# Optimization experiments

Hardware: AMD Instinct MI355X
Metric: run time of the kernel (lower is better)

## Reference

```python
import jax, jax.numpy as jnp
import numpy as np

N_BINS = 256
HOP = 80


def _gru(xs, Wih, Whh, bih, bhh, reverse=False):
    """Single-layer unidirectional GRU, PyTorch gate layout (r, z, n).
    xs: (T, B, I); Wih: (3H, I); Whh: (3H, H). Returns (T, B, H)."""
    H = Whh.shape[1]
    gi = jnp.einsum('tbi,gi->tbg', xs, Wih) + bih  # precompute input projections

    def step(h, gi_t):
        gh = h @ Whh.T + bhh
        ir, iz, inn = jnp.split(gi_t, 3, axis=-1)
        hr, hz, hn = jnp.split(gh, 3, axis=-1)
        r = jax.nn.sigmoid(ir + hr)
        z = jax.nn.sigmoid(iz + hz)
        n = jnp.tanh(inn + r * hn)
        h_new = (1.0 - z) * n + z * h
        return h_new, h_new

    h0 = jnp.zeros((xs.shape[1], H), xs.dtype)
    _, ys = jax.lax.scan(step, h0, gi, reverse=reverse)
    return ys


def _quantize(w):
    # continuous [-1, 1] -> bin index in [0, N_BINS-1]
    return jnp.clip(jnp.floor((w + 1.0) * (N_BINS / 2)), 0, N_BINS - 1).astype(jnp.int32)


def _forward(x, y, p):
    # --- encode: 2-layer bidirectional GRU over mel frames ---
    c = x
    for l in ('m0', 'm1'):
        f = _gru(c, p[l + 'f_Wih'], p[l + 'f_Whh'], p[l + 'f_bih'], p[l + 'f_bhh'])
        bwd = _gru(c, p[l + 'b_Wih'], p[l + 'b_Whh'], p[l + 'b_bih'], p[l + 'b_bhh'], reverse=True)
        c = jnp.concatenate([f, bwd], axis=-1)  # (t_m, b, 2*dim_enc)
    # nearest-neighbor upsample in time (matches F.interpolate default 'nearest')
    c = jnp.repeat(c, HOP, axis=0)  # (t_w, b, 2*dim_enc)

    # --- teacher forcing: shift waveform right, vectorize via embedding ---
    b = x.shape[1]
    w = jnp.concatenate([jnp.zeros((1, b), y.dtype), y[:-1]], axis=0)
    e = p['E'][_quantize(w)]  # (t_w, b, dim_vec)

    # --- wav GRU + projection + GELU ---
    o = _gru(jnp.concatenate([e, c], axis=-1), p['w_Wih'], p['w_Whh'], p['w_bih'], p['w_bhh'])
    o = jax.nn.gelu(o @ p['Wp'].T + p['bp'], approximate=False)  # (t_w, b, dim_proj)

    # --- categorical neg log prob over quantized targets ---
    logits = o @ p['Wd'].T + p['bd']  # (t_w, b, N_BINS)
    logp = jax.nn.log_softmax(logits, axis=-1)
    tgt = _quantize(y)
    nll = -jnp.mean(jnp.take_along_axis(logp, tgt[..., None], axis=-1))
    return nll


def setup_inputs() -> dict:
    key = jax.random.key(0)
    ks = iter(jax.random.split(key, 64))

    def rn(shape, s=0.08):
        return jax.random.normal(next(ks), shape, jnp.float32) * s

    t_m, b, dm = 32, 4, 80
    de, dv, dd, dp = 128, 256, 896, 512
    d = {}
    d['x'] = jax.random.normal(next(ks), (t_m, b, dm), jnp.float32)
    d['y'] = jax.random.uniform(next(ks), (t_m * HOP, b), jnp.float32, minval=-1.0, maxval=1.0)
    for name, i in [('m0f', dm), ('m0b', dm), ('m1f', 2 * de), ('m1b', 2 * de)]:
        d[name + '_Wih'] = rn((3 * de, i))
        d[name + '_Whh'] = rn((3 * de, de))
        d[name + '_bih'] = rn((3 * de,))
        d[name + '_bhh'] = rn((3 * de,))
    d['w_Wih'] = rn((3 * dd, 2 * de + dv))
    d['w_Whh'] = rn((3 * dd, dd))
    d['w_bih'] = rn((3 * dd,))
    d['w_bhh'] = rn((3 * dd,))
    d['Wp'] = rn((dp, dd))
    d['bp'] = rn((dp,))
    d['E'] = rn((N_BINS, dv))
    d['Wd'] = rn((N_BINS, dp))
    d['bd'] = rn((N_BINS,))
    return d


def reference(x, y, m0f_Wih, m0f_Whh, m0f_bih, m0f_bhh, m0b_Wih, m0b_Whh, m0b_bih, m0b_bhh,
              m1f_Wih, m1f_Whh, m1f_bih, m1f_bhh, m1b_Wih, m1b_Whh, m1b_bih, m1b_bhh,
              w_Wih, w_Whh, w_bih, w_bhh, Wp, bp, E, Wd, bd):
    p = dict(m0f_Wih=m0f_Wih, m0f_Whh=m0f_Whh, m0f_bih=m0f_bih, m0f_bhh=m0f_bhh,
             m0b_Wih=m0b_Wih, m0b_Whh=m0b_Whh, m0b_bih=m0b_bih, m0b_bhh=m0b_bhh,
             m1f_Wih=m1f_Wih, m1f_Whh=m1f_Whh, m1f_bih=m1f_bih, m1f_bhh=m1f_bhh,
             m1b_Wih=m1b_Wih, m1b_Whh=m1b_Whh, m1b_bih=m1b_bih, m1b_bhh=m1b_bhh,
             w_Wih=w_Wih, w_Whh=w_Whh, w_bih=w_bih, w_bhh=w_bhh,
             Wp=Wp, bp=bp, E=E, Wd=Wd, bd=bd)
    return _forward(x, y, p)
```

## Files before the change

kernel.cpp:

```cpp
#include <hip/hip_runtime.h>
#include <stdint.h>
#include <math.h>

typedef __attribute__((ext_vector_type(8))) short bf16x8;
typedef __attribute__((ext_vector_type(4))) float f32x4;
typedef __attribute__((ext_vector_type(4))) unsigned int u32x4;

#define BATCH 4
#define T_M 32
#define DE 128
#define T_W 2560
#define NWG 56

__device__ __forceinline__ float b2f(unsigned short h) {
  return __uint_as_float(((unsigned int)h) << 16);
}
__device__ __forceinline__ unsigned short f2b(float f) {
  unsigned int u = __float_as_uint(f);
  u = u + 0x7fffu + ((u >> 16) & 1u);
  return (unsigned short)(u >> 16);
}
__device__ __forceinline__ float blo(unsigned int u){ return __uint_as_float(u << 16); }
__device__ __forceinline__ float bhi(unsigned int u){ return __uint_as_float(u & 0xffff0000u); }
__device__ __forceinline__ float sigm(float x){
  return __builtin_amdgcn_rcpf(1.f + __expf(-x));
}
__device__ __forceinline__ float tanh_fast(float x){
  float x2 = fminf(fmaxf(x + x, -30.f), 30.f);
  return 1.f - 2.f * __builtin_amdgcn_rcpf(__expf(x2) + 1.f);
}
__device__ __forceinline__ float gelu_exact(float x){ return 0.5f * x * (1.f + erff(x * 0.70710678118654752f)); }

__global__ __launch_bounds__(256) void k_prep(
    const float* __restrict__ wih, const float* __restrict__ wp,
    const float* __restrict__ wd, const float* __restrict__ e,
    const float* __restrict__ whh,
    unsigned short* __restrict__ wih_b, unsigned short* __restrict__ wp_b,
    unsigned short* __restrict__ wd_b, unsigned short* __restrict__ eb,
    unsigned short* __restrict__ whh_p)
{
  int idx = blockIdx.x * 256 + threadIdx.x;
  const int N0 = 2688 * 512, N1 = 512 * 896, N2 = 256 * 512, N3 = 256 * 256;
  if (idx < N0) { wih_b[idx] = f2b(wih[idx]); return; }
  idx -= N0;
  if (idx < N1) { wp_b[idx] = f2b(wp[idx]); return; }
  idx -= N1;
  if (idx < N2) { wd_b[idx] = f2b(wd[idx]); return; }
  idx -= N2;
  if (idx < N3) { eb[idx] = f2b(e[idx]); return; }
  idx -= N3;
  if (idx >= 224 * 28 * 512) return;
  int j    = idx & 7;
  int r16  = (idx >> 3) & 15;
  int quad = (idx >> 7) & 3;
  int kc   = (idx >> 9) % 28;
  int G    = (idx >> 9) / 28;
  unsigned short val = 0;
  if (r16 < 12) {
    int row = (r16 >> 2) * 896 + G * 4 + (r16 & 3);
    int col = kc * 32 + quad * 8 + j;
    val = f2b(whh[(size_t)row * 896 + col]);
  }
  whh_p[idx] = val;
}

__global__ __launch_bounds__(384) void k_gi_enc(
    const float* __restrict__ in, const float* __restrict__ Wih,
    const float* __restrict__ bih, float* __restrict__ out, int K)
{
  __shared__ float in_s[256];
  int tb = blockIdx.x;
  for (int i = threadIdx.x; i < K; i += 384) in_s[i] = in[tb * K + i];
  __syncthreads();
  int row = threadIdx.x;
  float acc = bih[row];
  const float* wr = Wih + row * K;
  for (int k = 0; k < K; k += 4) {
    float4 w = *(const float4*)(wr + k);
    float4 v = *(const float4*)(in_s + k);
    acc += w.x * v.x + w.y * v.y + w.z * v.z + w.w * v.w;
  }
  out[tb * 384 + row] = acc;
}

__global__ __launch_bounds__(512) void k_scan_enc(
    const float* __restrict__ gi_f, const float* __restrict__ gi_b,
    const float* __restrict__ whh_f, const float* __restrict__ bhh_f,
    const float* __restrict__ whh_b, const float* __restrict__ bhh_b,
    float* __restrict__ c_out, unsigned short* __restrict__ cb)
{
  const int dir = blockIdx.x, tid = threadIdx.x;
  const float* gi  = dir ? gi_b  : gi_f;
  const float* whh = dir ? whh_b : whh_f;
  const float* bhh = dir ? bhh_b : bhh_f;
  __shared__ unsigned short h_s[BATCH][DE + 8];
  __shared__ float gh_s[384][4];
  __shared__ float bhh_s[384];
  for (int i = tid; i < 384; i += 512) bhh_s[i] = bhh[i];
  for (int i = tid; i < BATCH * (DE + 8); i += 512) ((unsigned short*)h_s)[i] = 0;
  __syncthreads();
  for (int s = 0; s < T_M; ++s) {
    int t = dir ? (T_M - 1 - s) : s;
    #pragma unroll
    for (int k3 = 0; k3 < 3; ++k3) {
      int d = tid + 512 * k3;
      int row = d >> 2, b = d & 3;
      const float* wr = whh + row * DE;
      float acc = 0.f;
      for (int j = 0; j < DE; j += 8) {
        float4 w0 = *(const float4*)(wr + j);
        float4 w1 = *(const float4*)(wr + j + 4);
        uint4  hv = *(const uint4*)&h_s[b][j];
        acc += w0.x * blo(hv.x) + w0.y * bhi(hv.x) + w0.z * blo(hv.y) + w0.w * bhi(hv.y);
        acc += w1.x * blo(hv.z) + w1.y * bhi(hv.z) + w1.z * blo(hv.w) + w1.w * bhi(hv.w);
      }
      gh_s[row][b] = acc + bhh_s[row];
    }
    __syncthreads();
    {
      int u = tid >> 2, b = tid & 3;
      const float* git = gi + (t * BATCH + b) * 384;
      float r = sigm(git[u] + gh_s[u][b]);
      float z = sigm(git[DE + u] + gh_s[DE + u][b]);
      float n = tanh_fast(git[2 * DE + u] + r * gh_s[2 * DE + u][b]);
      float hold = b2f(h_s[b][u]);
      float hnew = (1.f - z) * n + z * hold;
      int oi = (t * BATCH + b) * 256 + dir * DE + u;
      c_out[oi] = hnew;
      if (cb) cb[oi] = f2b(hnew);
      h_s[b][u] = f2b(hnew);
    }
    __syncthreads();
  }
}

__global__ __launch_bounds__(256) void k_mgemm(
    const unsigned short* __restrict__ A, const unsigned short* __restrict__ B,
    const float* __restrict__ bias, void* __restrict__ C,
    int M, int N, int K, int act, int c_bf16, int swz, int afuse,
    const unsigned short* __restrict__ Eb, const unsigned short* __restrict__ c1b,
    const float* __restrict__ yw)
{
  __shared__ unsigned short As[128][40];
  __shared__ unsigned short Bs[128][40];
  const int tid = threadIdx.x;
  const int m0 = blockIdx.x * 128, n0 = blockIdx.y * 128;
  const int lane = tid & 63, wave = tid >> 6;
  const int wy = wave >> 1, wx = wave & 1;
  const int row16 = lane & 15, quad = lane >> 4;
  const int sr = tid >> 1, sc = (tid & 1) * 16;
  const unsigned short* arow0 = nullptr;
  const unsigned short* arow1 = nullptr;
  if (afuse) {
    int row = m0 + sr, tt = row >> 2, b = row & 3;
    float w = (tt == 0) ? 0.f : yw[(tt - 1) * 4 + b];
    int q = (int)floorf((w + 1.f) * 128.f);
    q = q < 0 ? 0 : (q > 255 ? 255 : q);
    arow0 = Eb + q * 256;
    arow1 = c1b + ((tt / 80) * 4 + b) * 256;
  }
  f32x4 acc[4][4] = {};
  for (int kt = 0; kt < K; kt += 32) {
    uint4 av, av2;
    if (afuse) {
      int kk = kt + sc;
      const unsigned short* src = (kk < 256) ? (arow0 + kk) : (arow1 + kk - 256);
      av  = *(const uint4*)src;
      av2 = *(const uint4*)(src + 8);
    } else {
      av  = *(const uint4*)(A + (size_t)(m0 + sr) * K + kt + sc);
      av2 = *(const uint4*)(A + (size_t)(m0 + sr) * K + kt + sc + 8);
    }
    uint4 bv  = *(const uint4*)(B + (size_t)(n0 + sr) * K + kt + sc);
    uint4 bv2 = *(const uint4*)(B + (size_t)(n0 + sr) * K + kt + sc + 8);
    __syncthreads();
    *(uint4*)&As[sr][sc] = av; *(uint4*)&As[sr][sc + 8] = av2;
    *(uint4*)&Bs[sr][sc] = bv; *(uint4*)&Bs[sr][sc + 8] = bv2;
    __syncthreads();
    bf16x8 af[4], bf[4];
    #pragma unroll
    for (int i = 0; i < 4; ++i) af[i] = *(const bf16x8*)&As[wy * 64 + i * 16 + row16][quad * 8];
    #pragma unroll
    for (int j = 0; j < 4; ++j) bf[j] = *(const bf16x8*)&Bs[wx * 64 + j * 16 + row16][quad * 8];
    #pragma unroll
    for (int i = 0; i < 4; ++i)
      #pragma unroll
      for (int j = 0; j < 4; ++j)
        acc[i][j] = __builtin_amdgcn_mfma_f32_16x16x32_bf16(af[i], bf[j], acc[i][j], 0, 0, 0);
  }
  #pragma unroll
  for (int i = 0; i < 4; ++i) {
    #pragma unroll
    for (int j = 0; j < 4; ++j) {
      int col = n0 + wx * 64 + j * 16 + row16;
      float bs = bias[col];
      #pragma unroll
      for (int r = 0; r < 4; ++r) {
        int row = m0 + wy * 64 + i * 16 + quad * 4 + r;
        float v = acc[i][j][r] + bs;
        if (act) v = gelu_exact(v);
        if (swz) {
          int t = row >> 2, b = row & 3;
          int g = col / 896, rem = col - g * 896;
          int G = rem >> 2, u = rem & 3;
          ((unsigned short*)C)[(size_t)(t * 224 + G) * 48 + g * 16 + b * 4 + u] = f2b(v);
        } else if (c_bf16) {
          ((unsigned short*)C)[(size_t)row * N + col] = f2b(v);
        } else {
          ((float*)C)[(size_t)row * N + col] = v;
        }
      }
    }
  }
}

__global__ __launch_bounds__(256, 1) void k_wav_rnn(
    const unsigned short* __restrict__ whh_p,
    const float* __restrict__ bhh,
    const unsigned short* __restrict__ gp_,
    unsigned int* __restrict__ hslots,
    unsigned int* __restrict__ O32)
{
  const int wg = blockIdx.x, tid = threadIdx.x;
  const int lane = tid & 63, wave = tid >> 6;
  const int G = wg * 4 + wave;

  __shared__ unsigned short h_lds[2][4][912];
  __shared__ float phh[4][3][4][4];

  const int r16 = lane & 15, quad = lane >> 4, bb = lane & 3;
  const int fu = (lane >> 2) & 3, fb = lane & 3;

  bf16x8 wf[28];
  {
    const bf16x8* W8 = (const bf16x8*)whh_p + (size_t)G * 28 * 64;
    #pragma unroll
    for (int kc = 0; kc < 28; ++kc)
      wf[kc] = W8[(kc * 4 + quad) * 16 + r16];
  }

  const float br_ = bhh[G * 4 + fu];
  const float bz_ = bhh[896 + G * 4 + fu];
  const float bn_ = bhh[1792 + G * 4 + fu];
  float hprev = 0.f;
  const unsigned short* gl0 = gp_ + (size_t)G * 48 + fb * 4 + fu;
  unsigned short cr = gl0[0], cz = gl0[16], cn = gl0[32];

  const int p0 = tid, p1 = tid + 256, p2 = tid + 512;
  const int p3 = (tid < 128) ? tid + 768 : tid;
  const int pb0 = p0 / 224, pG0 = p0 - pb0 * 224;
  const int pb1 = p1 / 224, pG1 = p1 - pb1 * 224;
  const int pb2 = p2 / 224, pG2 = p2 - pb2 * 224;
  const int pb3 = p3 / 224, pG3 = p3 - pb3 * 224;

  const unsigned long long base0 = (unsigned long long)hslots;
  const unsigned long long base1 = base0 + 14336ull;

  for (int t = 0; t < T_W; ++t) {
    const unsigned long long hb = (t & 1) ? base1 : base0;
    unsigned long long a0 = hb + ((unsigned long long)p0 << 4);
    unsigned long long a1 = hb + ((unsigned long long)p1 << 4);
    unsigned long long a2 = hb + ((unsigned long long)p2 << 4);
    unsigned long long a3 = hb + ((unsigned long long)p3 << 4);
    u32x4 s0, s1, s2, s3;
    const unsigned int tg = (unsigned int)t;
    for (;;) {
      asm volatile(
        "global_load_dwordx4 %0, %4, off sc0 sc1\n"
        "global_load_dwordx4 %1, %5, off sc0 sc1\n"
        "global_load_dwordx4 %2, %6, off sc0 sc1\n"
        "global_load_dwordx4 %3, %7, off sc0 sc1\n"
        "s_waitcnt vmcnt(0)"
        : "=&v"(s0), "=&v"(s1), "=&v"(s2), "=&v"(s3)
        : "v"(a0), "v"(a1), "v"(a2), "v"(a3)
        : "memory");
      unsigned int bad = (s0.z ^ tg) | (s1.z ^ tg) | (s2.z ^ tg) | (s3.z ^ tg);
      if (!__any(bad != 0)) break;
    }

    int tn = (t + 1 < T_W) ? (t + 1) : t;
    const unsigned short* gp = gp_ + (size_t)tn * 10752 + G * 48 + fb * 4 + fu;
    unsigned short nr_ = gp[0], nz_ = gp[16], nn_ = gp[32];

    *(uint2*)&h_lds[t & 1][pb0][pG0 * 4] = make_uint2(s0.x, s0.y);
    *(uint2*)&h_lds[t & 1][pb1][pG1 * 4] = make_uint2(s1.x, s1.y);
    *(uint2*)&h_lds[t & 1][pb2][pG2 * 4] = make_uint2(s2.x, s2.y);
    *(uint2*)&h_lds[t & 1][pb3][pG3 * 4] = make_uint2(s3.x, s3.y);
    __syncthreads();

    f32x4 ac0 = {}, ac1 = {}, ac2 = {}, ac3 = {};
    #pragma unroll
    for (int kc = 0; kc < 28; kc += 4) {
      bf16x8 h0 = *(const bf16x8*)&h_lds[t & 1][bb][(kc + 0) * 32 + quad * 8];
      bf16x8 h1 = *(const bf16x8*)&h_lds[t & 1][bb][(kc + 1) * 32 + quad * 8];
      bf16x8 h2 = *(const bf16x8*)&h_lds[t & 1][bb][(kc + 2) * 32 + quad * 8];
      bf16x8 h3 = *(const bf16x8*)&h_lds[t & 1][bb][(kc + 3) * 32 + quad * 8];
      ac0 = __builtin_amdgcn_mfma_f32_16x16x32_bf16(wf[kc + 0], h0, ac0, 0, 0, 0);
      ac1 = __builtin_amdgcn_mfma_f32_16x16x32_bf16(wf[kc + 1], h1, ac1, 0, 0, 0);
      ac2 = __builtin_amdgcn_mfma_f32_16x16x32_bf16(wf[kc + 2], h2, ac2, 0, 0, 0);
      ac3 = __builtin_amdgcn_mfma_f32_16x16x32_bf16(wf[kc + 3], h3, ac3, 0, 0, 0);
    }
    f32x4 ac;
    ac[0] = ac0[0] + ac1[0] + ac2[0] + ac3[0];
    ac[1] = ac0[1] + ac1[1] + ac2[1] + ac3[1];
    ac[2] = ac0[2] + ac1[2] + ac2[2] + ac3[2];
    ac[3] = ac0[3] + ac1[3] + ac2[3] + ac3[3];

    if (r16 < 4 && quad < 3)
      *(f32x4*)&phh[wave][quad][r16][0] = ac;
    asm volatile("s_waitcnt lgkmcnt(0)" ::: "memory");

    float pr = phh[wave][0][fb][fu];
    float pz = phh[wave][1][fb][fu];
    float pn = phh[wave][2][fb][fu];
    float r = sigm(b2f(cr) + br_ + pr);
    float z = sigm(b2f(cz) + bz_ + pz);
    float n = tanh_fast(b2f(cn) + bn_ + r * pn);
    float h = (1.f - z) * n + z * hprev;
    hprev = h;
    unsigned int hu = f2b(h);
    cr = nr_; cz = nz_; cn = nn_;

    int b = lane & 3;
    unsigned int u0v = (unsigned int)__shfl((int)hu, 0 + b);
    unsigned int u1v = (unsigned int)__shfl((int)hu, 4 + b);
    unsigned int u2v = (unsigned int)__shfl((int)hu, 8 + b);
    unsigned int u3v = (unsigned int)__shfl((int)hu, 12 + b);
    if (lane < 4) {
      u32x4 pkt;
      pkt.x = (u0v & 0xffffu) | (u1v << 16);
      pkt.y = (u2v & 0xffffu) | (u3v << 16);
      pkt.z = (unsigned int)(t + 1);
      pkt.w = 0u;
      unsigned long long sa = (((t + 1) & 1) ? base1 : base0)
                            + (unsigned long long)((b * 224 + G) << 4);
      asm volatile("global_store_dwordx4 %0, %1, off sc0 sc1"
                   :: "v"(sa), "v"(pkt) : "memory");
      *(uint2*)(O32 + (size_t)(t * 4 + b) * 448 + G * 2) = make_uint2(pkt.x, pkt.y);
    }
  }
}

__global__ __launch_bounds__(256) void k_nll(
    const float* __restrict__ logits, const float* __restrict__ y,
    float* __restrict__ partials)
{
  __shared__ float ps[4];
  int wid = threadIdx.x >> 6, lane = threadIdx.x & 63;
  int row = blockIdx.x * 4 + wid;
  const float* lr = logits + (size_t)row * 256;
  float v0 = lr[lane], v1 = lr[lane + 64], v2 = lr[lane + 128], v3 = lr[lane + 192];
  float mx = fmaxf(fmaxf(v0, v1), fmaxf(v2, v3));
  for (int off = 32; off > 0; off >>= 1) mx = fmaxf(mx, __shfl_xor(mx, off));
  float se = __expf(v0 - mx) + __expf(v1 - mx) + __expf(v2 - mx) + __expf(v3 - mx);
  for (int off = 32; off > 0; off >>= 1) se += __shfl_xor(se, off);
  if (lane == 0) {
    float w = y[row];
    int q = (int)floorf((w + 1.f) * 128.f);
    q = q < 0 ? 0 : (q > 255 ? 255 : q);
    ps[wid] = (logf(se) + mx) - lr[q];
  }
  __syncthreads();
  if (threadIdx.x == 0) partials[blockIdx.x] = ps[0] + ps[1] + ps[2] + ps[3];
}

__global__ __launch_bounds__(256) void k_final(const float* __restrict__ partials,
                                               float* __restrict__ out)
{
  __shared__ float s[4];
  int tid = threadIdx.x;
  float a = 0.f;
  for (int i = tid; i < 2560; i += 256) a += partials[i];
  for (int off = 32; off > 0; off >>= 1) a += __shfl_xor(a, off);
  if ((tid & 63) == 0) s[tid >> 6] = a;
  __syncthreads();
  if (tid == 0) out[0] = (s[0] + s[1] + s[2] + s[3]) * (1.f / 10240.f);
}

extern "C" void kernel_launch(void* const* d_in, const int* in_sizes, int n_in,
                              void* d_out, int out_size, void* d_ws, size_t ws_size,
                              hipStream_t stream)
{
  const float* x       = (const float*)d_in[0];
  const float* y       = (const float*)d_in[1];
  const float* m0f_Wih = (const float*)d_in[2];
  const float* m0f_Whh = (const float*)d_in[3];
  const float* m0f_bih = (const float*)d_in[4];
  const float* m0f_bhh = (const float*)d_in[5];
  const float* m0b_Wih = (const float*)d_in[6];
  const float* m0b_Whh = (const float*)d_in[7];
  const float* m0b_bih = (const float*)d_in[8];
  const float* m0b_bhh = (const float*)d_in[9];
  const float* m1f_Wih = (const float*)d_in[10];
  const float* m1f_Whh = (const float*)d_in[11];
  const float* m1f_bih = (const float*)d_in[12];
  const float* m1f_bhh = (const float*)d_in[13];
  const float* m1b_Wih = (const float*)d_in[14];
  const float* m1b_Whh = (const float*)d_in[15];
  const float* m1b_bih = (const float*)d_in[16];
  const float* m1b_bhh = (const float*)d_in[17];
  const float* w_Wih   = (const float*)d_in[18];
  const float* w_Whh   = (const float*)d_in[19];
  const float* w_bih   = (const float*)d_in[20];
  const float* w_bhh   = (const float*)d_in[21];
  const float* Wp      = (const float*)d_in[22];
  const float* bp      = (const float*)d_in[23];
  const float* E       = (const float*)d_in[24];
  const float* Wd      = (const float*)d_in[25];
  const float* bd      = (const float*)d_in[26];

  char* ws = (char*)d_ws;
  size_t off = 0;
  auto alloc = [&](size_t bytes) -> void* {
    void* p = ws + off;
    off += (bytes + 255) & ~(size_t)255;
    return p;
  };
  unsigned int* hslots = (unsigned int*)alloc(2 * 896 * 16);
  size_t misc_bytes = off;

  float* c0   = (float*)alloc((size_t)32 * 4 * 256 * 4);
  float* c1   = (float*)alloc((size_t)32 * 4 * 256 * 4);
  float* gi0f = (float*)alloc((size_t)32 * 4 * 384 * 4);
  float* gi0b = (float*)alloc((size_t)32 * 4 * 384 * 4);
  float* gi1f = (float*)alloc((size_t)32 * 4 * 384 * 4);
  float* gi1b = (float*)alloc((size_t)32 * 4 * 384 * 4);
  unsigned short* Eb    = (unsigned short*)alloc((size_t)256 * 256 * 2);
  unsigned short* c1b   = (unsigned short*)alloc((size_t)32 * 4 * 256 * 2);
  unsigned short* gpack = (unsigned short*)alloc((size_t)2560 * 224 * 48 * 2);
  unsigned int*   O32   = (unsigned int*)alloc((size_t)10240 * 448 * 4);
  unsigned short* O2    = (unsigned short*)alloc((size_t)10240 * 512 * 2);
  float*          LG    = (float*)alloc((size_t)10240 * 256 * 4);
  float*          PT    = (float*)alloc((size_t)2560 * 4);
  unsigned short* Wih_b = (unsigned short*)alloc((size_t)2688 * 512 * 2);
  unsigned short* Whh_p = (unsigned short*)alloc((size_t)224 * 28 * 512 * 2);
  unsigned short* Wp_b  = (unsigned short*)alloc((size_t)512 * 896 * 2);
  unsigned short* Wd_b  = (unsigned short*)alloc((size_t)256 * 512 * 2);

  hipMemsetAsync(d_ws, 0, misc_bytes, stream);

  {
    int total = 2688 * 512 + 512 * 896 + 256 * 512 + 256 * 256 + 224 * 28 * 512;
    k_prep<<<(total + 255) / 256, 256, 0, stream>>>(
        w_Wih, Wp, Wd, E, w_Whh, Wih_b, Wp_b, Wd_b, Eb, Whh_p);
  }

  k_gi_enc<<<128, 384, 0, stream>>>(x, m0f_Wih, m0f_bih, gi0f, 80);
  k_gi_enc<<<128, 384, 0, stream>>>(x, m0b_Wih, m0b_bih, gi0b, 80);
  k_scan_enc<<<2, 512, 0, stream>>>(gi0f, gi0b, m0f_Whh, m0f_bhh, m0b_Whh, m0b_bhh,
                                    c0, nullptr);
  k_gi_enc<<<128, 384, 0, stream>>>(c0, m1f_Wih, m1f_bih, gi1f, 256);
  k_gi_enc<<<128, 384, 0, stream>>>(c0, m1b_Wih, m1b_bih, gi1b, 256);
  k_scan_enc<<<2, 512, 0, stream>>>(gi1f, gi1b, m1f_Whh, m1f_bhh, m1b_Whh, m1b_bhh,
                                    c1, c1b);

  k_mgemm<<<dim3(80, 21), 256, 0, stream>>>(nullptr, Wih_b, w_bih, (void*)gpack,
                                            10240, 2688, 512, 0, 1, 1, 1, Eb, c1b, y);

  k_wav_rnn<<<NWG, 256, 0, stream>>>(Whh_p, w_bhh, gpack, hslots, O32);

  k_mgemm<<<dim3(80, 4), 256, 0, stream>>>((const unsigned short*)O32, Wp_b, bp,
                                           (void*)O2, 10240, 512, 896, 1, 1, 0, 0,
                                           nullptr, nullptr, nullptr);
  k_mgemm<<<dim3(80, 2), 256, 0, stream>>>(O2, Wd_b, bd, (void*)LG,
                                           10240, 256, 512, 0, 0, 0, 0,
                                           nullptr, nullptr, nullptr);
  k_nll<<<2560, 256, 0, stream>>>(LG, y, PT);
  k_final<<<1, 256, 0, stream>>>(PT, (float*)d_out);
}
```

Baseline: 5.765 ms.

## Stage GEMM epilogue through LDS for coalesced stores and re-layout gate pack

The bf16 GEMM epilogue now writes results into a shared-memory tile and then emits 16-byte coalesced global stores, instead of scattered 2-byte stores. The gate-projection pack layout changes from [t][G][48] to [t][gate][G][16], which makes the swizzled stores contiguous, and the recurrent kernel's gate loads are updated to match. The two encoder input-projection launches per layer are merged into one 2D grid. The trade-off is a 34KB extra LDS buffer per GEMM block, which may lower occupancy, plus an extra barrier.

Result: no change. 5.776 ms (+0.2%).

```diff
diff --git a/kernel.cpp b/kernel.cpp
--- a/kernel.cpp
+++ b/kernel.cpp
@@ -64,12 +64,17 @@
   whh_p[idx] = val;
 }
 
-__global__ __launch_bounds__(384) void k_gi_enc(
-    const float* __restrict__ in, const float* __restrict__ Wih,
-    const float* __restrict__ bih, float* __restrict__ out, int K)
+__global__ __launch_bounds__(384) void k_gi_enc2(
+    const float* __restrict__ in,
+    const float* __restrict__ Wih_f, const float* __restrict__ bih_f,
+    const float* __restrict__ Wih_b, const float* __restrict__ bih_b,
+    float* __restrict__ out_f, float* __restrict__ out_b, int K)
 {
   __shared__ float in_s[256];
   int tb = blockIdx.x;
+  const float* Wih = blockIdx.y ? Wih_b : Wih_f;
+  const float* bih = blockIdx.y ? bih_b : bih_f;
+  float* out       = blockIdx.y ? out_b : out_f;
   for (int i = threadIdx.x; i < K; i += 384) in_s[i] = in[tb * K + i];
   __syncthreads();
   int row = threadIdx.x;
@@ -143,6 +148,7 @@
 {
   __shared__ unsigned short As[128][40];
   __shared__ unsigned short Bs[128][40];
+  __shared__ unsigned short Cs[128][136];
   const int tid = threadIdx.x;
   const int m0 = blockIdx.x * 128, n0 = blockIdx.y * 128;
   const int lane = tid & 63, wave = tid >> 6;
@@ -188,25 +194,62 @@
       for (int j = 0; j < 4; ++j)
         acc[i][j] = __builtin_amdgcn_mfma_f32_16x16x32_bf16(af[i], bf[j], acc[i][j], 0, 0, 0);
   }
-  #pragma unroll
-  for (int i = 0; i < 4; ++i) {
-    #pragma unroll
-    for (int j = 0; j < 4; ++j) {
-      int col = n0 + wx * 64 + j * 16 + row16;
-      float bs = bias[col];
+
+  if (swz || c_bf16) {
+    #pragma unroll
+    for (int i = 0; i < 4; ++i) {
       #pragma unroll
-      for (int r = 0; r < 4; ++r) {
-        int row = m0 + wy * 64 + i * 16 + quad * 4 + r;
-        float v = acc[i][j][r] + bs;
-        if (act) v = gelu_exact(v);
-        if (swz) {
-          int t = row >> 2, b = row & 3;
-          int g = col / 896, rem = col - g * 896;
-          int G = rem >> 2, u = rem & 3;
-          ((unsigned short*)C)[(size_t)(t * 224 + G) * 48 + g * 16 + b * 4 + u] = f2b(v);
-        } else if (c_bf16) {
-          ((unsigned short*)C)[(size_t)row * N + col] = f2b(v);
-        } else {
+      for (int j = 0; j < 4; ++j) {
+        int col = n0 + wx * 64 + j * 16 + row16;
+        float bs = bias[col];
+        #pragma unroll
+        for (int r = 0; r < 4; ++r) {
+          float v = acc[i][j][r] + bs;
+          if (act) v = gelu_exact(v);
+          Cs[wy * 64 + i * 16 + quad * 4 + r][wx * 64 + j * 16 + row16] = f2b(v);
+        }
+      }
+    }
+    __syncthreads();
+    if (swz) {
+      int g = n0 / 896, G0 = (n0 - g * 896) >> 2;
+      unsigned short* gout = (unsigned short*)C;
+      #pragma unroll
+      for (int k = 0; k < 4; ++k) {
+        int bid = tid + 256 * k;
+        int tt = bid >> 5, Gl = bid & 31;
+        uint2 q0 = *(const uint2*)&Cs[tt * 4 + 0][Gl * 4];
+        uint2 q1 = *(const uint2*)&Cs[tt * 4 + 1][Gl * 4];
+        uint2 q2 = *(const uint2*)&Cs[tt * 4 + 2][Gl * 4];
+        uint2 q3 = *(const uint2*)&Cs[tt * 4 + 3][Gl * 4];
+        size_t di = ((size_t)(((m0 >> 2) + tt) * 3 + g) * 224 + (G0 + Gl)) * 16;
+        *(uint4*)&gout[di]     = make_uint4(q0.x, q0.y, q1.x, q1.y);
+        *(uint4*)&gout[di + 8] = make_uint4(q2.x, q2.y, q3.x, q3.y);
+      }
+    } else {
+      unsigned short* co = (unsigned short*)C;
+      #pragma unroll
+      for (int k = 0; k < 4; ++k) {
+        int idx = tid + 256 * k;
+        int row = idx >> 3, c16 = (idx & 7) * 16;
+        uint4 a = *(const uint4*)&Cs[row][c16];
+        uint4 b = *(const uint4*)&Cs[row][c16 + 8];
+        *(uint4*)&co[(size_t)(m0 + row) * N + n0 + c16]     = a;
+        *(uint4*)&co[(size_t)(m0 + row) * N + n0 + c16 + 8] = b;
+      }
+    }
+  } else {
+    #pragma unroll
+    for (int i = 0; i < 4; ++i) {
+      #pragma unroll
+      for (int j = 0; j < 4; ++j) {
+        int col = n0 + wx * 64 + j * 16 + row16;
+        float bs = bias[col];
+        #pragma unroll
+        for (int r = 0; r < 4; ++r) {
+          int row = m0 + wy * 64 + i * 16 + quad * 4 + r;
+          float v = acc[i][j][r] + bs;
+          if (act) v = gelu_exact(v);
           ((float*)C)[(size_t)row * N + col] = v;
         }
       }
@@ -243,8 +286,8 @@
   const float bz_ = bhh[896 + G * 4 + fu];
   const float bn_ = bhh[1792 + G * 4 + fu];
   float hprev = 0.f;
-  const unsigned short* gl0 = gp_ + (size_t)G * 48 + fb * 4 + fu;
-  unsigned short cr = gl0[0], cz = gl0[16], cn = gl0[32];
+  const unsigned short* gl0 = gp_ + (size_t)G * 16 + fb * 4 + fu;
+  unsigned short cr = gl0[0], cz = gl0[3584], cn = gl0[7168];
 
   const int p0 = tid, p1 = tid + 256, p2 = tid + 512;
   const int p3 = (tid < 128) ? tid + 768 : tid;
@@ -279,8 +322,8 @@
     }
 
     int tn = (t + 1 < T_W) ? (t + 1) : t;
-    const unsigned short* gp = gp_ + (size_t)tn * 10752 + G * 48 + fb * 4 + fu;
-    unsigned short nr_ = gp[0], nz_ = gp[16], nn_ = gp[32];
+    const unsigned short* gp = gp_ + (size_t)tn * 10752 + G * 16 + fb * 4 + fu;
+    unsigned short nr_ = gp[0], nz_ = gp[3584], nn_ = gp[7168];
 
     *(uint2*)&h_lds[t & 1][pb0][pG0 * 4] = make_uint2(s0.x, s0.y);
     *(uint2*)&h_lds[t & 1][pb1][pG1 * 4] = make_uint2(s1.x, s1.y);
@@ -427,7 +470,7 @@
   float* gi1b = (float*)alloc((size_t)32 * 4 * 384 * 4);
   unsigned short* Eb    = (unsigned short*)alloc((size_t)256 * 256 * 2);
   unsigned short* c1b   = (unsigned short*)alloc((size_t)32 * 4 * 256 * 2);
-  unsigned short* gpack = (unsigned short*)alloc((size_t)2560 * 224 * 48 * 2);
+  unsigned short* gpack = (unsigned short*)alloc((size_t)2560 * 3 * 224 * 16 * 2);
   unsigned int*   O32   = (unsigned int*)alloc((size_t)10240 * 448 * 4);
   unsigned short* O2    = (unsigned short*)alloc((size_t)10240 * 512 * 2);
   float*          LG    = (float*)alloc((size_t)10240 * 256 * 4);
@@ -445,12 +488,12 @@
         w_Wih, Wp, Wd, E, w_Whh, Wih_b, Wp_b, Wd_b, Eb, Whh_p);
   }
 
-  k_gi_enc<<<128, 384, 0, stream>>>(x, m0f_Wih, m0f_bih, gi0f, 80);
-  k_gi_enc<<<128, 384, 0, stream>>>(x, m0b_Wih, m0b_bih, gi0b, 80);
+  k_gi_enc2<<<dim3(128, 2), 384, 0, stream>>>(x, m0f_Wih, m0f_bih, m0b_Wih, m0b_bih,
+                                              gi0f, gi0b, 80);
   k_scan_enc<<<2, 512, 0, stream>>>(gi0f, gi0b, m0f_Whh, m0f_bhh, m0b_Whh, m0b_bhh,
                                     c0, nullptr);
-  k_gi_enc<<<128, 384, 0, stream>>>(c0, m1f_Wih, m1f_bih, gi1f, 256);
-  k_gi_enc<<<128, 384, 0, stream>>>(c0, m1b_Wih, m1b_bih, gi1b, 256);
+  k_gi_enc2<<<dim3(128, 2), 384, 0, stream>>>(c0, m1f_Wih, m1f_bih, m1b_Wih, m1b_bih,
+                                              gi1f, gi1b, 256);
   k_scan_enc<<<2, 512, 0, stream>>>(gi1f, gi1b, m1f_Whh, m1f_bhh, m1b_Whh, m1b_bhh,
                                     c1, c1b);
 
```
